# Optimization experiments

Measured on AMD Instinct MI355X. Metric: run time of the kernel, lower is better.

Reference implementation:

```python
import jax, jax.numpy as jnp
import numpy as np

B, N, K, C, H, W = 2, 8, 8, 256, 96, 96
CTX = C + K + 4 * K + 13  # 309
HID = 256
ALPHA = 0.3          # REFINE_EMA_ALPHA
TEMP = 1.0           # READOUT_TEMPERATURE
SIM_HIGH, SIM_LOW = 0.8, 0.3
A_KEEP, A_REFINE, A_REPLACE, A_SPAWN = 0, 1, 2, 3


def _l2norm(x, axis=-1, eps=1e-12):
    return x / jnp.maximum(jnp.linalg.norm(x, axis=axis, keepdims=True), eps)


def setup_inputs() -> dict:
    key = jax.random.key(0)
    ks = jax.random.split(key, 12)
    value = jax.random.normal(ks[0], (B, N, C, H, W), jnp.float32)
    frame_feat = jax.random.normal(ks[1], (B, C, H, W), jnp.float32)
    mask = jax.random.uniform(ks[2], (B, N, H, W), jnp.float32)
    proto = jax.random.normal(ks[3], (B, N, K, C), jnp.float32)
    age = jax.random.uniform(ks[4], (B, N, K), jnp.float32) * 10.0
    usage = jax.random.uniform(ks[5], (B, N, K), jnp.float32) * 5.0
    conf = jax.random.uniform(ks[6], (B, N, K), jnp.float32)
    valid = jax.random.randint(ks[7], (B, N, K), 0, 2).astype(bool)
    W1 = jax.random.normal(ks[8], (CTX, HID), jnp.float32) * 0.02
    b1 = jnp.zeros((HID,), jnp.float32)
    W2 = jax.random.normal(ks[9], (HID, 4), jnp.float32) * 0.02
    b2 = jnp.zeros((4,), jnp.float32)
    proto_gate = jnp.float32(1.0)
    frame_gate = jnp.float32(1.0)
    return dict(value=value, frame_feat=frame_feat, mask=mask, proto=proto,
                age=age, usage=usage, conf=conf, W1=W1, b1=b1, W2=W2, b2=b2,
                proto_gate=proto_gate, frame_gate=frame_gate, valid=valid)


def reference(value, frame_feat, mask, proto, age, usage, conf,
              W1, b1, W2, b2, proto_gate, frame_gate, valid):
    # ---- candidate prototype via masked pooling (PROTO_POOLING='mask') ----
    fv = value.reshape(B, N, C, H * W)                      # [B,N,C,HW]
    fm = mask.reshape(B, N, 1, H * W)                       # [B,N,1,HW]
    denom = jnp.maximum(fm.sum(-1), 1e-6)                   # [B,N,1]
    cand = (fv * fm).sum(-1) / denom                        # [B,N,C]
    mask_strength = fm.mean(-1)[..., 0]                     # [B,N]
    fallback = fv.mean(-1)
    cand = jnp.where((denom[..., 0] <= 1e-5)[..., None], fallback, cand)
    cand = _l2norm(cand)

    # ---- uncertainty features (prev_mask is None -> temporal term = 0) ----
    m = jnp.clip(mask, 1e-4, 1.0 - 1e-4)
    ent = -(m * jnp.log(m) + (1.0 - m) * jnp.log(1.0 - m))
    fg_prob = m.mean((-2, -1))
    fg_area = (m > 0.5).astype(jnp.float32).mean((-2, -1))
    gx = jnp.abs(m[..., 1:, :] - m[..., :-1, :]).mean((-2, -1))
    gy = jnp.abs(m[..., :, 1:] - m[..., :, :-1]).mean((-2, -1))
    unc = jnp.stack([ent.mean((-2, -1)), fg_prob, fg_area,
                     0.5 * (gx + gy), jnp.zeros_like(fg_prob)], -1)  # [B,N,5]

    # ---- context / similarity ----
    bank_n = _l2norm(proto)                                  # [B,N,K,C]
    sim = jnp.einsum('bnc,bnkc->bnk', cand, bank_n)
    sim = jnp.where(valid, sim, -1.0)
    g_t = jnp.broadcast_to(frame_feat.mean((2, 3))[:, None, :], (B, N, C))
    age_n = age / jnp.maximum(age.max(), 1.0)
    usage_n = usage / jnp.maximum(usage.max(), 1.0)
    bank_stats = jnp.stack([valid.astype(jnp.float32), age_n, usage_n, conf], -1)
    top2 = jax.lax.top_k(sim, 2)[0]
    t1, t2 = top2[..., 0], top2[..., 1]
    glob = jnp.stack([valid.astype(jnp.float32).mean(-1), age_n.max(-1),
                      usage_n.min(-1), conf.mean(-1), conf.max(-1)], -1)
    context = jnp.concatenate([g_t, sim, bank_stats.reshape(B, N, 4 * K),
                               jnp.stack([t1, t2, t1 - t2], -1), glob, unc], -1)
    logits = jax.nn.gelu(context @ W1 + b1, approximate=False) @ W2 + b2  # [B,N,4]

    any_valid = valid.any(-1)
    target_slot = jnp.where(any_valid, sim.argmax(-1), 0)
    max_sim = jnp.take_along_axis(sim, target_slot[..., None], -1)[..., 0]
    max_sim = jnp.where(any_valid, max_sim, -1.0)

    # ---- rule-based action selection ----
    action = jnp.where(~any_valid, A_SPAWN,
             jnp.where(max_sim >= SIM_HIGH, A_REFINE,
             jnp.where(max_sim >= SIM_LOW, A_KEEP, A_SPAWN)))

    # ---- victim / slot selection ----
    victim = (age_n + (1.0 - usage_n) + (1.0 - conf)).argmax(-1)
    first_empty = (~valid).argmax(-1)
    spawn_slot = jnp.where((~valid).any(-1), first_empty, victim)
    upd_slot = jnp.where(action == A_REFINE, target_slot, spawn_slot)

    # ---- policy-gated EMA scatter update of the bank ----
    onehot = jax.nn.one_hot(upd_slot, K, dtype=bool)                 # [B,N,K]
    refine_m = onehot & (action == A_REFINE)[..., None]
    write_m = onehot & (action == A_SPAWN)[..., None]
    refined = _l2norm((1.0 - ALPHA) * proto + ALPHA * cand[:, :, None, :])
    cand_b = jnp.broadcast_to(cand[:, :, None, :], proto.shape)
    proto_new = jnp.where(refine_m[..., None], refined,
                jnp.where(write_m[..., None], cand_b, proto))
    upd_m = refine_m | write_m
    age_new = jnp.where(upd_m, 0.0, age + 1.0)
    usage_new = usage + upd_m.astype(jnp.float32)
    conf_new = jnp.where(write_m, mask_strength[..., None],
               jnp.where(refine_m, jnp.maximum(conf, max_sim[..., None]), conf))
    valid_new = valid | write_m

    # ---- prototype-conditioned readout ----
    bank_nn = _l2norm(proto_new)                                      # [B,N,K,C]
    vn = value / jnp.maximum(jnp.linalg.norm(value, axis=2, keepdims=True), 1e-12)
    rsim = jnp.einsum('bnkc,bnchw->bnkhw', bank_nn, vn)
    rlog = jnp.where(valid_new[..., None, None], rsim / TEMP, -1e9)
    attn = jax.nn.softmax(rlog, axis=2)
    attn = attn * valid_new.any(-1)[..., None, None, None].astype(jnp.float32)
    proto_map = jnp.einsum('bnkhw,bnkc->bnchw', attn, proto_new)
    conditioned = value + proto_gate * proto_map + frame_gate * frame_feat[:, None]
    return conditioned
```

## Files before the change

### kernel.cpp

```cpp
#include <hip/hip_runtime.h>
#include <math.h>

constexpr int Bc = 2, Nc = 8, Kc = 8, Cc = 256, HWc = 96 * 96;
constexpr int BN = Bc * Nc;
constexpr int HW2 = HWc / 2;
constexpr float ALPHA = 0.3f;
constexpr float SIM_HIGH = 0.8f, SIM_LOW = 0.3f;
constexpr int TILES = 72;

__device__ __forceinline__ float wred_sum_all(float v) {
#pragma unroll
  for (int o = 32; o > 0; o >>= 1) v += __shfl_xor(v, o, 64);
  return v;
}
__device__ __forceinline__ float wred_sum(float v) {
#pragma unroll
  for (int o = 32; o > 0; o >>= 1) v += __shfl_down(v, o, 64);
  return v;
}
__device__ __forceinline__ float wred_max(float v) {
#pragma unroll
  for (int o = 32; o > 0; o >>= 1) v = fmaxf(v, __shfl_down(v, o, 64));
  return v;
}
__device__ __forceinline__ float bred_sum(float v, float* sc) {
  int lane = threadIdx.x & 63, wid = threadIdx.x >> 6;
  v = wred_sum(v);
  __syncthreads();
  if (lane == 0) sc[wid] = v;
  __syncthreads();
  return sc[0] + sc[1] + sc[2] + sc[3];
}
__device__ __forceinline__ float bred_max(float v, float* sc) {
  int lane = threadIdx.x & 63, wid = threadIdx.x >> 6;
  v = wred_max(v);
  __syncthreads();
  if (lane == 0) sc[wid] = v;
  __syncthreads();
  return fmaxf(fmaxf(sc[0], sc[1]), fmaxf(sc[2], sc[3]));
}

__device__ __forceinline__ float lane_bcast(float x, int c0) {
  return __int_as_float(__builtin_amdgcn_readlane(__float_as_int(x), c0));
}

__global__ __launch_bounds__(256) void k1_sums(const float* __restrict__ value,
                                               const float* __restrict__ mask,
                                               float* __restrict__ sum_v,
                                               float* __restrict__ sum_vm) {
  const int bnc = blockIdx.x;
  const int bn = bnc >> 8;
  const int tid = threadIdx.x;
  const float4* v4 = (const float4*)(value + (size_t)bnc * HWc);
  const float4* m4 = (const float4*)(mask + (size_t)bn * HWc);
  float av = 0.f, avm = 0.f;
#pragma unroll
  for (int i = 0; i < 9; ++i) {
    float4 v = v4[i * 256 + tid];
    float4 m = m4[i * 256 + tid];
    av += v.x + v.y + v.z + v.w;
    avm += v.x * m.x + v.y * m.y + v.z * m.z + v.w * m.w;
  }
  __shared__ float sc[8];
  float rv = wred_sum(av);
  float rvm = wred_sum(avm);
  int lane = tid & 63, wid = tid >> 6;
  if (lane == 0) { sc[wid] = rv; sc[4 + wid] = rvm; }
  __syncthreads();
  if (tid == 0) {
    sum_v[bnc] = sc[0] + sc[1] + sc[2] + sc[3];
    sum_vm[bnc] = sc[4] + sc[5] + sc[6] + sc[7];
  }
}

__global__ __launch_bounds__(256) void k2_update(
    const float* __restrict__ mask, const float* __restrict__ proto,
    const float* __restrict__ age, const float* __restrict__ usage,
    const float* __restrict__ conf, const int* __restrict__ valid,
    const float* __restrict__ sum_v, const float* __restrict__ sum_vm,
    float* __restrict__ proto_new, float* __restrict__ bank_inv,
    float* __restrict__ validf) {
  const int bn = blockIdx.x;
  const int tid = threadIdx.x;
  const int lane = tid & 63, w = tid >> 6;
  __shared__ float sc[4];
  __shared__ float s_cand[Cc];
  __shared__ float s_sim[Kc];
  __shared__ int s_slot, s_ref, s_wr;

  float a = (tid < BN * Kc) ? age[tid] : -3e38f;
  float u = (tid < BN * Kc) ? usage[tid] : -3e38f;
  const float age_den = fmaxf(bred_max(a, sc), 1.0f);
  const float usage_den = fmaxf(bred_max(u, sc), 1.0f);

  float ms = 0.f;
  const float4* m4 = (const float4*)(mask + (size_t)bn * HWc);
  for (int i = tid; i < HWc / 4; i += 256) {
    const float4 mm = m4[i];
    ms += (mm.x + mm.y) + (mm.z + mm.w);
  }
  const float msum = bred_sum(ms, sc);
  const float denom = fmaxf(msum, 1e-6f);

  const int c = tid;
  const float sv = sum_v[bn * Cc + c];
  const float svm = sum_vm[bn * Cc + c];
  float cand = (denom <= 1e-5f) ? (sv * (1.0f / HWc)) : (svm / denom);
  const float css = bred_sum(cand * cand, sc);
  s_cand[c] = cand / fmaxf(sqrtf(css), 1e-12f);
  __syncthreads();

  const float4* cand4 = (const float4*)s_cand;
  const float4 c4 = cand4[lane];

#pragma unroll
  for (int kk = 0; kk < 2; ++kk) {
    const int k = w + kk * 4;
    const float4 p4 = ((const float4*)(proto + ((size_t)bn * Kc + k) * Cc))[lane];
    const float pss = wred_sum_all(p4.x * p4.x + p4.y * p4.y + p4.z * p4.z + p4.w * p4.w);
    const float pd  = wred_sum_all(p4.x * c4.x + p4.y * c4.y + p4.z * c4.z + p4.w * c4.w);
    if (lane == 0)
      s_sim[k] = (valid[bn * Kc + k] != 0) ? (pd / fmaxf(sqrtf(pss), 1e-12f)) : -1.0f;
  }
  __syncthreads();

  if (tid == 0) {
    bool anyv = false;
    for (int k = 0; k < Kc; ++k) anyv = anyv || (valid[bn * Kc + k] != 0);
    int tslot = 0; float best = s_sim[0];
    for (int k = 1; k < Kc; ++k)
      if (s_sim[k] > best) { best = s_sim[k]; tslot = k; }
    const float max_sim = anyv ? best : -1.0f;
    const int action = (!anyv) ? 3 : (max_sim >= SIM_HIGH ? 1 : (max_sim >= SIM_LOW ? 0 : 3));
    int victim = 0; float vb = -3e38f;
    for (int k = 0; k < Kc; ++k) {
      const float s = age[bn * Kc + k] / age_den + (1.f - usage[bn * Kc + k] / usage_den) +
                      (1.f - conf[bn * Kc + k]);
      if (s > vb) { vb = s; victim = k; }
    }
    int fe = 0; bool hasE = false;
    for (int k = 0; k < Kc; ++k)
      if (valid[bn * Kc + k] == 0) { fe = k; hasE = true; break; }
    const int spawn = hasE ? fe : victim;
    s_slot = (action == 1) ? tslot : spawn;
    s_ref = (action == 1);
    s_wr = (action == 3);
  }
  __syncthreads();

#pragma unroll
  for (int kk = 0; kk < 2; ++kk) {
    const int k = w + kk * 4;
    const float4 p4 = ((const float4*)(proto + ((size_t)bn * Kc + k) * Cc))[lane];
    float4 pn;
    if (k == s_slot && s_ref) {
      float4 t;
      t.x = (1.0f - ALPHA) * p4.x + ALPHA * c4.x;
      t.y = (1.0f - ALPHA) * p4.y + ALPHA * c4.y;
      t.z = (1.0f - ALPHA) * p4.z + ALPHA * c4.z;
      t.w = (1.0f - ALPHA) * p4.w + ALPHA * c4.w;
      const float tss = wred_sum_all(t.x * t.x + t.y * t.y + t.z * t.z + t.w * t.w);
      const float inv = 1.0f / fmaxf(sqrtf(tss), 1e-12f);
      pn.x = t.x * inv; pn.y = t.y * inv; pn.z = t.z * inv; pn.w = t.w * inv;
    } else if (k == s_slot && s_wr) {
      pn = c4;
    } else {
      pn = p4;
    }
    ((float4*)(proto_new + ((size_t)bn * Kc + k) * Cc))[lane] = pn;
    const float bss = wred_sum_all(pn.x * pn.x + pn.y * pn.y + pn.z * pn.z + pn.w * pn.w);
    if (lane == 0) bank_inv[bn * Kc + k] = 1.0f / fmaxf(sqrtf(bss), 1e-12f);
  }
  if (tid < Kc) {
    const int k = tid;
    const int vn = (valid[bn * Kc + k] != 0) || (s_wr && k == s_slot);
    validf[bn * Kc + k] = vn ? 1.0f : 0.0f;
  }
}

__global__ __launch_bounds__(256, 8) void k3_readout(
    const float* __restrict__ value, const float* __restrict__ frame,
    const float* __restrict__ proto_new, const float* __restrict__ bank_inv,
    const float* __restrict__ validf, const float* __restrict__ pgp,
    const float* __restrict__ fgp, float* __restrict__ out) {
  const int bn = blockIdx.x / TILES;
  const int tile = blockIdx.x % TILES;
  const int b = bn >> 3;
  const int tid = threadIdx.x;
  const int lane = tid & 63, w = tid >> 6;
  const int p2 = tile * 64 + lane;

  __shared__ float s_part[4 * 9 * 128];

  const float* psrc = proto_new + (size_t)bn * Kc * Cc + w * 64 + lane;
  float pnr[8];
#pragma unroll
  for (int k = 0; k < 8; ++k) pnr[k] = psrc[k * Cc];

  const float pg = pgp[0], fg = fgp[0];
  const float2* v2 = (const float2*)(value + (size_t)bn * Cc * HWc);
  const float2* f2 = (const float2*)(frame + (size_t)b * Cc * HWc);
  float2* o2 = (float2*)(out + (size_t)bn * Cc * HWc);

  float ss0 = 0.f, ss1 = 0.f;
  float d0[8], d1[8];
#pragma unroll
  for (int k = 0; k < 8; ++k) { d0[k] = 0.f; d1[k] = 0.f; }

#pragma unroll 8
  for (int c0 = 0; c0 < 64; ++c0) {
    const float2 v = v2[(size_t)(w * 64 + c0) * HW2 + p2];
    ss0 += v.x * v.x; ss1 += v.y * v.y;
#pragma unroll
    for (int k = 0; k < 8; ++k) {
      const float pk = lane_bcast(pnr[k], c0);
      d0[k] += pk * v.x;
      d1[k] += pk * v.y;
    }
  }

  float2* sp2 = (float2*)s_part;
#pragma unroll
  for (int k = 0; k < 8; ++k)
    sp2[(w * 9 + k) * 64 + lane] = make_float2(d0[k], d1[k]);
  sp2[(w * 9 + 8) * 64 + lane] = make_float2(ss0, ss1);
  __syncthreads();

  float a0[8], a1[8];
  {
    float dd0[9], dd1[9];
#pragma unroll
    for (int j = 0; j < 9; ++j) {
      const float2 t0 = sp2[(0 * 9 + j) * 64 + lane];
      const float2 t1 = sp2[(1 * 9 + j) * 64 + lane];
      const float2 t2 = sp2[(2 * 9 + j) * 64 + lane];
      const float2 t3 = sp2[(3 * 9 + j) * 64 + lane];
      dd0[j] = (t0.x + t1.x) + (t2.x + t3.x);
      dd1[j] = (t0.y + t1.y) + (t2.y + t3.y);
    }
    const float rn0 = 1.0f / fmaxf(sqrtf(dd0[8]), 1e-12f);
    const float rn1 = 1.0f / fmaxf(sqrtf(dd1[8]), 1e-12f);
    float m0 = -3e38f, m1 = -3e38f;
    float vldk[8];
#pragma unroll
    for (int k = 0; k < 8; ++k) {
      vldk[k] = validf[bn * Kc + k];
      const float sc = bank_inv[bn * Kc + k];
      dd0[k] *= sc * rn0;
      dd1[k] *= sc * rn1;
      if (vldk[k] > 0.5f) { m0 = fmaxf(m0, dd0[k]); m1 = fmaxf(m1, dd1[k]); }
    }
    float sum0 = 0.f, sum1 = 0.f;
#pragma unroll
    for (int k = 0; k < 8; ++k) {
      a0[k] = (vldk[k] > 0.5f) ? __expf(dd0[k] - m0) : 0.f;
      a1[k] = (vldk[k] > 0.5f) ? __expf(dd1[k] - m1) : 0.f;
      sum0 += a0[k]; sum1 += a1[k];
    }
    const float i0 = (sum0 > 0.f) ? 1.0f / sum0 : 0.f;
    const float i1 = (sum1 > 0.f) ? 1.0f / sum1 : 0.f;
#pragma unroll
    for (int k = 0; k < 8; ++k) { a0[k] *= i0; a1[k] *= i1; }
  }

#pragma unroll 4
  for (int c0 = 0; c0 < 64; ++c0) {
    const size_t off = (size_t)(w * 64 + c0) * HW2 + p2;
    const float2 v = v2[off];
    const float2 f = f2[off];
    float pm0 = 0.f, pm1 = 0.f;
#pragma unroll
    for (int k = 0; k < 8; ++k) {
      const float pk = lane_bcast(pnr[k], c0);
      pm0 += a0[k] * pk;
      pm1 += a1[k] * pk;
    }
    float2 o;
    o.x = v.x + pg * pm0 + fg * f.x;
    o.y = v.y + pg * pm1 + fg * f.y;
    o2[off] = o;
  }
}

extern "C" void kernel_launch(void* const* d_in, const int* in_sizes, int n_in,
                              void* d_out, int out_size, void* d_ws, size_t ws_size,
                              hipStream_t stream) {
  const float* value = (const float*)d_in[0];
  const float* frame = (const float*)d_in[1];
  const float* mask  = (const float*)d_in[2];
  const float* proto = (const float*)d_in[3];
  const float* age   = (const float*)d_in[4];
  const float* usage = (const float*)d_in[5];
  const float* conf  = (const float*)d_in[6];
  const float* pg = (const float*)d_in[11];
  const float* fg = (const float*)d_in[12];
  const int* valid = (const int*)d_in[13];
  float* out = (float*)d_out;

  float* w = (float*)d_ws;
  float* sum_v     = w;
  float* sum_vm    = w + 4096;
  float* proto_new = w + 8192;
  float* bank_inv  = w + 40960;
  float* validf    = w + 41088;

  hipLaunchKernelGGL(k1_sums, dim3(BN * Cc), dim3(256), 0, stream,
                     value, mask, sum_v, sum_vm);
  hipLaunchKernelGGL(k2_update, dim3(BN), dim3(256), 0, stream,
                     mask, proto, age, usage, conf, valid, sum_v, sum_vm,
                     proto_new, bank_inv, validf);
  hipLaunchKernelGGL(k3_readout, dim3(BN * TILES), dim3(256), 0, stream,
                     value, frame, proto_new, bank_inv, validf, pg, fg, out);
}
```

Baseline: 354.0 us.

## Fuse prototype update into readout kernel and compute mask sum in pooling kernel

Removes the single-block-per-bn update kernel by having every readout block redundantly recompute the prototype update decision and new bank in shared memory. The mask sum moves into the first pooling kernel, so the update stage no longer rereads the mask. This saves a launch and a serialized low-parallelism stage, plus the global round-trip of proto_new. In exchange each of the 72 tiles per bn repeats the small update work, and shared memory use grows through a union that could reduce occupancy.

New measurement: 357.0 us. Within noise of the previous version (+0.9%).

```diff
diff --git a/kernel.cpp b/kernel.cpp
--- a/kernel.cpp
+++ b/kernel.cpp
@@ -47,89 +47,95 @@
 __global__ __launch_bounds__(256) void k1_sums(const float* __restrict__ value,
                                                const float* __restrict__ mask,
                                                float* __restrict__ sum_v,
-                                               float* __restrict__ sum_vm) {
+                                               float* __restrict__ sum_vm,
+                                               float* __restrict__ msum) {
   const int bnc = blockIdx.x;
   const int bn = bnc >> 8;
   const int tid = threadIdx.x;
   const float4* v4 = (const float4*)(value + (size_t)bnc * HWc);
   const float4* m4 = (const float4*)(mask + (size_t)bn * HWc);
-  float av = 0.f, avm = 0.f;
+  float av = 0.f, avm = 0.f, am = 0.f;
 #pragma unroll
   for (int i = 0; i < 9; ++i) {
     float4 v = v4[i * 256 + tid];
     float4 m = m4[i * 256 + tid];
     av += v.x + v.y + v.z + v.w;
     avm += v.x * m.x + v.y * m.y + v.z * m.z + v.w * m.w;
-  }
-  __shared__ float sc[8];
+    am += (m.x + m.y) + (m.z + m.w);
+  }
+  __shared__ float sc[12];
   float rv = wred_sum(av);
   float rvm = wred_sum(avm);
+  float rm = wred_sum(am);
   int lane = tid & 63, wid = tid >> 6;
-  if (lane == 0) { sc[wid] = rv; sc[4 + wid] = rvm; }
+  if (lane == 0) { sc[wid] = rv; sc[4 + wid] = rvm; sc[8 + wid] = rm; }
   __syncthreads();
   if (tid == 0) {
     sum_v[bnc] = sc[0] + sc[1] + sc[2] + sc[3];
     sum_vm[bnc] = sc[4] + sc[5] + sc[6] + sc[7];
-  }
-}
-
-__global__ __launch_bounds__(256) void k2_update(
-    const float* __restrict__ mask, const float* __restrict__ proto,
+    if ((bnc & 255) == 0)
+      msum[bn] = sc[8] + sc[9] + sc[10] + sc[11];
+  }
+}
+
+__global__ __launch_bounds__(256, 8) void k3_fused(
+    const float* __restrict__ value, const float* __restrict__ frame,
+    const float* __restrict__ mask_unused, const float* __restrict__ proto,
     const float* __restrict__ age, const float* __restrict__ usage,
     const float* __restrict__ conf, const int* __restrict__ valid,
     const float* __restrict__ sum_v, const float* __restrict__ sum_vm,
-    float* __restrict__ proto_new, float* __restrict__ bank_inv,
-    float* __restrict__ validf) {
-  const int bn = blockIdx.x;
+    const float* __restrict__ msum, const float* __restrict__ pgp,
+    const float* __restrict__ fgp, float* __restrict__ out) {
+  const int bn = blockIdx.x / TILES;
+  const int tile = blockIdx.x % TILES;
+  const int b = bn >> 3;
   const int tid = threadIdx.x;
   const int lane = tid & 63, w = tid >> 6;
+  const int p2 = tile * 64 + lane;
+
+  __shared__ union {
+    struct { float cand[Cc]; float pn[Kc * Cc]; float sim[Kc]; } pre;
+    float part[4 * 9 * 128];
+  } u;
   __shared__ float sc[4];
-  __shared__ float s_cand[Cc];
-  __shared__ float s_sim[Kc];
+  __shared__ float s_binv[Kc], s_vld[Kc];
   __shared__ int s_slot, s_ref, s_wr;
 
   float a = (tid < BN * Kc) ? age[tid] : -3e38f;
-  float u = (tid < BN * Kc) ? usage[tid] : -3e38f;
+  float uu = (tid < BN * Kc) ? usage[tid] : -3e38f;
   const float age_den = fmaxf(bred_max(a, sc), 1.0f);
-  const float usage_den = fmaxf(bred_max(u, sc), 1.0f);
-
-  float ms = 0.f;
-  const float4* m4 = (const float4*)(mask + (size_t)bn * HWc);
-  for (int i = tid; i < HWc / 4; i += 256) {
-    const float4 mm = m4[i];
-    ms += (mm.x + mm.y) + (mm.z + mm.w);
-  }
-  const float msum = bred_sum(ms, sc);
-  const float denom = fmaxf(msum, 1e-6f);
-
-  const int c = tid;
-  const float sv = sum_v[bn * Cc + c];
-  const float svm = sum_vm[bn * Cc + c];
+  const float usage_den = fmaxf(bred_max(uu, sc), 1.0f);
+
+  const float denom = fmaxf(msum[bn], 1e-6f);
+
+  const float sv = sum_v[bn * Cc + tid];
+  const float svm = sum_vm[bn * Cc + tid];
   float cand = (denom <= 1e-5f) ? (sv * (1.0f / HWc)) : (svm / denom);
   const float css = bred_sum(cand * cand, sc);
-  s_cand[c] = cand / fmaxf(sqrtf(css), 1e-12f);
-  __syncthreads();
-
-  const float4* cand4 = (const float4*)s_cand;
-  const float4 c4 = cand4[lane];
-
+  u.pre.cand[tid] = cand / fmaxf(sqrtf(css), 1e-12f);
+  __syncthreads();
+
+  const float4 c4 = ((const float4*)u.pre.cand)[lane];
+
+  float4 p4k[2];
 #pragma unroll
   for (int kk = 0; kk < 2; ++kk) {
     const int k = w + kk * 4;
-    const float4 p4 = ((const float4*)(proto + ((size_t)bn * Kc + k) * Cc))[lane];
+    p4k[kk] = ((const float4*)(proto + ((size_t)bn * Kc + k) * Cc))[lane];
+    const float4 p4 = p4k[kk];
     const float pss = wred_sum_all(p4.x * p4.x + p4.y * p4.y + p4.z * p4.z + p4.w * p4.w);
     const float pd  = wred_sum_all(p4.x * c4.x + p4.y * c4.y + p4.z * c4.z + p4.w * c4.w);
     if (lane == 0)
-      s_sim[k] = (valid[bn * Kc + k] != 0) ? (pd / fmaxf(sqrtf(pss), 1e-12f)) : -1.0f;
+      u.pre.sim[k] = (valid[bn * Kc + k] != 0) ? (pd / fmaxf(sqrtf(pss), 1e-12f)) : -1.0f;
   }
   __syncthreads();
 
   if (tid == 0) {
     bool anyv = false;
     for (int k = 0; k < Kc; ++k) anyv = anyv || (valid[bn * Kc + k] != 0);
-    int tslot = 0; float best = s_sim[0];
+    int tslot = 0; float best = u.pre.sim[0];
     for (int k = 1; k < Kc; ++k)
-      if (s_sim[k] > best) { best = s_sim[k]; tslot = k; }
+      if (u.pre.sim[k] > best) { best = u.pre.sim[k]; tslot = k; }
     const float max_sim = anyv ? best : -1.0f;
     const int action = (!anyv) ? 3 : (max_sim >= SIM_HIGH ? 1 : (max_sim >= SIM_LOW ? 0 : 3));
     int victim = 0; float vb = -3e38f;
@@ -151,7 +157,7 @@
 #pragma unroll
   for (int kk = 0; kk < 2; ++kk) {
     const int k = w + kk * 4;
-    const float4 p4 = ((const float4*)(proto + ((size_t)bn * Kc + k) * Cc))[lane];
+    const float4 p4 = p4k[kk];
     float4 pn;
     if (k == s_slot && s_ref) {
       float4 t;
@@ -167,35 +173,22 @@
     } else {
       pn = p4;
     }
-    ((float4*)(proto_new + ((size_t)bn * Kc + k) * Cc))[lane] = pn;
+    ((float4*)(u.pre.pn + k * Cc))[lane] = pn;
     const float bss = wred_sum_all(pn.x * pn.x + pn.y * pn.y + pn.z * pn.z + pn.w * pn.w);
-    if (lane == 0) bank_inv[bn * Kc + k] = 1.0f / fmaxf(sqrtf(bss), 1e-12f);
-  }
-  if (tid < Kc) {
-    const int k = tid;
-    const int vn = (valid[bn * Kc + k] != 0) || (s_wr && k == s_slot);
-    validf[bn * Kc + k] = vn ? 1.0f : 0.0f;
-  }
-}
-
-__global__ __launch_bounds__(256, 8) void k3_readout(
-    const float* __restrict__ value, const float* __restrict__ frame,
-    const float* __restrict__ proto_new, const float* __restrict__ bank_inv,
-    const float* __restrict__ validf, const float* __restrict__ pgp,
-    const float* __restrict__ fgp, float* __restrict__ out) {
-  const int bn = blockIdx.x / TILES;
-  const int tile = blockIdx.x % TILES;
-  const int b = bn >> 3;
-  const int tid = threadIdx.x;
-  const int lane = tid & 63, w = tid >> 6;
-  const int p2 = tile * 64 + lane;
-
-  __shared__ float s_part[4 * 9 * 128];
-
-  const float* psrc = proto_new + (size_t)bn * Kc * Cc + w * 64 + lane;
-  float pnr[8];
-#pragma unroll
-  for (int k = 0; k < 8; ++k) pnr[k] = psrc[k * Cc];
+    if (lane == 0) s_binv[k] = 1.0f / fmaxf(sqrtf(bss), 1e-12f);
+  }
+  if (tid < Kc)
+    s_vld[tid] = ((valid[bn * Kc + tid] != 0) || (s_wr && tid == s_slot)) ? 1.0f : 0.0f;
+  __syncthreads();
+
+  float pnr[8], binv[8], vld[8];
+#pragma unroll
+  for (int k = 0; k < 8; ++k) {
+    pnr[k] = u.pre.pn[k * Cc + w * 64 + lane];
+    binv[k] = s_binv[k];
+    vld[k] = s_vld[k];
+  }
+  __syncthreads();
 
   const float pg = pgp[0], fg = fgp[0];
   const float2* v2 = (const float2*)(value + (size_t)bn * Cc * HWc);
@@ -219,7 +212,7 @@
     }
   }
 
-  float2* sp2 = (float2*)s_part;
+  float2* sp2 = (float2*)u.part;
 #pragma unroll
   for (int k = 0; k < 8; ++k)
     sp2[(w * 9 + k) * 64 + lane] = make_float2(d0[k], d1[k]);
@@ -241,20 +234,18 @@
     const float rn0 = 1.0f / fmaxf(sqrtf(dd0[8]), 1e-12f);
     const float rn1 = 1.0f / fmaxf(sqrtf(dd1[8]), 1e-12f);
     float m0 = -3e38f, m1 = -3e38f;
-    float vldk[8];
 #pragma unroll
     for (int k = 0; k < 8; ++k) {
-      vldk[k] = validf[bn * Kc + k];
-      const float sc = bank_inv[bn * Kc + k];
-      dd0[k] *= sc * rn0;
-      dd1[k] *= sc * rn1;
-      if (vldk[k] > 0.5f) { m0 = fmaxf(m0, dd0[k]); m1 = fmaxf(m1, dd1[k]); }
+      const float scl = binv[k];
+      dd0[k] *= scl * rn0;
+      dd1[k] *= scl * rn1;
+      if (vld[k] > 0.5f) { m0 = fmaxf(m0, dd0[k]); m1 = fmaxf(m1, dd1[k]); }
     }
     float sum0 = 0.f, sum1 = 0.f;
 #pragma unroll
     for (int k = 0; k < 8; ++k) {
-      a0[k] = (vldk[k] > 0.5f) ? __expf(dd0[k] - m0) : 0.f;
-      a1[k] = (vldk[k] > 0.5f) ? __expf(dd1[k] - m1) : 0.f;
+      a0[k] = (vld[k] > 0.5f) ? __expf(dd0[k] - m0) : 0.f;
+      a1[k] = (vld[k] > 0.5f) ? __expf(dd1[k] - m1) : 0.f;
       sum0 += a0[k]; sum1 += a1[k];
     }
     const float i0 = (sum0 > 0.f) ? 1.0f / sum0 : 0.f;
@@ -298,17 +289,13 @@
   float* out = (float*)d_out;
 
   float* w = (float*)d_ws;
-  float* sum_v     = w;
-  float* sum_vm    = w + 4096;
-  float* proto_new = w + 8192;
-  float* bank_inv  = w + 40960;
-  float* validf    = w + 41088;
+  float* sum_v  = w;
+  float* sum_vm = w + 4096;
+  float* msum   = w + 8192;
 
   hipLaunchKernelGGL(k1_sums, dim3(BN * Cc), dim3(256), 0, stream,
-                     value, mask, sum_v, sum_vm);
-  hipLaunchKernelGGL(k2_update, dim3(BN), dim3(256), 0, stream,
-                     mask, proto, age, usage, conf, valid, sum_v, sum_vm,
-                     proto_new, bank_inv, validf);
-  hipLaunchKernelGGL(k3_readout, dim3(BN * TILES), dim3(256), 0, stream,
-                     value, frame, proto_new, bank_inv, validf, pg, fg, out);
-}
+                     value, mask, sum_v, sum_vm, msum);
+  hipLaunchKernelGGL(k3_fused, dim3(BN * TILES), dim3(256), 0, stream,
+                     value, frame, mask, proto, age, usage, conf, valid,
+                     sum_v, sum_vm, msum, pg, fg, out);
+}
```
